# Kernel tuning notes

Hardware: AMD Instinct MI355X
Metric: run time of the kernel (lower is better)

## Reference

```python
import jax, jax.numpy as jnp
import numpy as np

B, S, D, HD, M, NH, DFF = 32, 512, 512, 512, 1000, 8, 2048
BETA = 0.5
DH = D // NH


def _make_seq(kt, km):
    # sorted event times, integer markers stored as floats (as in torch code);
    # last quarter of each sequence is padding with sentinel t = -1, marker = -1
    t = jnp.sort(jax.random.uniform(kt, (B, S)) * 100.0, axis=1)
    mk = jax.random.randint(km, (B, S), 0, M).astype(jnp.float32)
    valid = jnp.arange(S) < (3 * S // 4)
    t = jnp.where(valid, t, -1.0)
    mk = jnp.where(valid, mk, -1.0)
    return jnp.stack([t, mk], axis=-1)  # [B, S, 2]


def setup_inputs() -> dict:
    key = jax.random.key(0)
    ks = jax.random.split(key, 20)
    s = 0.02
    n = lambda k, shp: jax.random.normal(k, shp, dtype=jnp.float32) * s
    return {
        'x_H': _make_seq(ks[0], ks[1]),
        'x_F': _make_seq(ks[2], ks[3]),
        'W_m': n(ks[4], (D, M)),
        'W_t': n(ks[5], (D,)),
        'b_t': n(ks[6], (D,)),
        'Wq': n(ks[7], (D, D)),
        'Wk': n(ks[8], (D, D)),
        'Wv': n(ks[9], (D, D)),
        'Wo': n(ks[10], (D, D)),
        'W1': n(ks[11], (D, DFF)),
        'b1': jnp.zeros((DFF,), jnp.float32),
        'W2': n(ks[12], (DFF, D)),
        'b2': jnp.zeros((D,), jnp.float32),
        'Wp': n(ks[13], (D, HD)),
        'bp': jnp.zeros((HD,), jnp.float32),
        'W_out': n(ks[14], (2 * HD, M)),
        'b_out': jnp.zeros((M,), jnp.float32),
    }


def _embed(x, W_m, W_t, b_t):
    # out = beta * W_m[:, marker] + (1-beta) * (W_t * t + b_t); zeros when t < 0
    t = x[..., 0]                                         # [B, S]
    mk = jnp.clip(x[..., 1], 0, M - 1).astype(jnp.int32)  # [B, S]
    e = BETA * W_m.T[mk] + (1.0 - BETA) * (W_t * t[..., None] + b_t)
    return jnp.where((t >= 0)[..., None], e, 0.0), (t >= 0)


def _encoder(e, mask, Wq, Wk, Wv, Wo, W1, b1, W2, b2, Wp, bp):
    # masked multi-head self-attention encoder + masked mean pool -> [B, HD]
    q = (e @ Wq).reshape(B, S, NH, DH)
    k = (e @ Wk).reshape(B, S, NH, DH)
    v = (e @ Wv).reshape(B, S, NH, DH)
    scores = jnp.einsum('bqhd,bkhd->bhqk', q, k) / (DH ** 0.5)
    scores = jnp.where(mask[:, None, None, :], scores, -1e9)
    a = jax.nn.softmax(scores, axis=-1)
    o = jnp.einsum('bhqk,bkhd->bqhd', a, v).reshape(B, S, D) @ Wo
    h = e + o
    h = h + jax.nn.relu(h @ W1 + b1) @ W2 + b2
    mf = mask.astype(e.dtype)[..., None]
    pooled = (h * mf).sum(axis=1) / jnp.maximum(mf.sum(axis=1), 1.0)
    return pooled @ Wp + bp


def reference(x_H, x_F, W_m, W_t, b_t, Wq, Wk, Wv, Wo, W1, b1, W2, b2, Wp, bp, W_out, b_out):
    eH, mH = _embed(x_H, W_m, W_t, b_t)
    eF, mF = _embed(x_F, W_m, W_t, b_t)
    hH = _encoder(eH, mH, Wq, Wk, Wv, Wo, W1, b1, W2, b2, Wp, bp)
    hF = _encoder(eF, mF, Wq, Wk, Wv, Wo, W1, b1, W2, b2, Wp, bp)
    lam = jax.nn.softmax(jnp.concatenate([hH, hF], axis=1) @ W_out + b_out, axis=1)
    mu = jnp.argmax(lam, axis=1)
    return lam, mu
```

## Files before the change

kernel.cpp:

```cpp
#include <hip/hip_runtime.h>
#include <math.h>

#define BATCH 32
#define BB    64
#define SEQ  512
#define DIM  512
#define MM   1000
#define NHEAD 8
#define DHEAD 64
#define DFFN 2048
#define BROWS (BB * SEQ)

typedef __attribute__((ext_vector_type(8))) short short8;
typedef __attribute__((ext_vector_type(4))) float f32x4;

__device__ __forceinline__ ushort f2bf(float x) {
    unsigned u = __builtin_bit_cast(unsigned, x);
    unsigned r = (u + 0x7FFFu + ((u >> 16) & 1u)) >> 16;
    return (ushort)r;
}
__device__ __forceinline__ float bf2f(ushort h) {
    unsigned u = ((unsigned)h) << 16;
    return __builtin_bit_cast(float, u);
}

#define GL2LDS(g, s) __builtin_amdgcn_global_load_lds( \
    (const __attribute__((address_space(1))) unsigned int*)(g), \
    (__attribute__((address_space(3))) unsigned int*)(s), 16, 0, 0)

constexpr size_t OFF_WMT  = 0;
constexpr size_t OFF_MASK = 524288;
constexpr size_t OFF_POOL = 557056;
constexpr size_t OFF_HENC = 589824;
constexpr size_t OFF_LOG  = 622592;
constexpr size_t OFF_WQTH = 655360;
constexpr size_t OFF_W1TH = 1179648;
constexpr size_t OFF_W2TH = 1703936;
constexpr size_t OFF_EHI  = 2228224;
constexpr size_t OFF_ELO  = 10616832;
constexpr size_t OFF_QB   = 19005440;
constexpr size_t OFF_KB   = 27394048;
constexpr size_t OFF_VB   = 35782656;

__global__ __launch_bounds__(256)
void transpose_wm(const float* __restrict__ Wm, float* __restrict__ WmT)
{
    __shared__ float tile[32][33];
    int tx = threadIdx.x & 31;
    int ty = threadIdx.x >> 5;
    int mx = blockIdx.x * 32;
    int dy = blockIdx.y * 32;
    for (int i = ty; i < 32; i += 8) {
        int d = dy + i, m = mx + tx;
        tile[i][tx] = (m < MM) ? Wm[(size_t)d * MM + m] : 0.f;
    }
    __syncthreads();
    for (int i = ty; i < 32; i += 8) {
        int m = mx + i, d = dy + tx;
        if (m < MM) WmT[(size_t)m * DIM + d] = tile[tx][i];
    }
}

__global__ __launch_bounds__(256)
void split_wT4(const float* __restrict__ Wq, const float* __restrict__ Wk,
               const float* __restrict__ Wv, const float* __restrict__ Wo,
               ushort* __restrict__ Th)
{
    __shared__ float tile[32][33];
    int tx = threadIdx.x & 31;
    int ty = threadIdx.x >> 5;
    int n0 = blockIdx.x * 32;
    int k0 = blockIdx.y * 32;
    const float* W = (n0 < 512) ? Wq : (n0 < 1024) ? Wk
                   : (n0 < 1536) ? Wv : Wo;
    int nc = n0 & 511;
    for (int i = ty; i < 32; i += 8)
        tile[i][tx] = W[(size_t)(k0 + i) * 512 + nc + tx];
    __syncthreads();
    for (int i = ty; i < 32; i += 8)
        Th[(size_t)(n0 + i) * 512 + k0 + tx] = f2bf(tile[tx][i]);
}

__global__ __launch_bounds__(256)
void split_wT(const float* __restrict__ W, ushort* __restrict__ Th, int K, int N)
{
    __shared__ float tile[32][33];
    int tx = threadIdx.x & 31;
    int ty = threadIdx.x >> 5;
    int n0 = blockIdx.x * 32;
    int k0 = blockIdx.y * 32;
    for (int i = ty; i < 32; i += 8)
        tile[i][tx] = W[(size_t)(k0 + i) * N + n0 + tx];
    __syncthreads();
    for (int i = ty; i < 32; i += 8)
        Th[(size_t)(n0 + i) * K + k0 + tx] = f2bf(tile[tx][i]);
}

__global__ __launch_bounds__(256)
void embed_kernel(const float* __restrict__ xH, const float* __restrict__ xF,
                  const float* __restrict__ WmT, const float* __restrict__ Wt,
                  const float* __restrict__ bt,
                  ushort* __restrict__ ehi, ushort* __restrict__ elo,
                  float* __restrict__ maskA)
{
    int sub  = threadIdx.x >> 6;
    int lane = threadIdx.x & 63;
    int bs   = blockIdx.x * 4 + sub;
    const float* xp = (bs < BATCH * SEQ) ? (xH + (size_t)bs * 2)
                                         : (xF + (size_t)(bs - BATCH * SEQ) * 2);
    float t   = xp[0];
    float mkf = xp[1];
    int   mk  = (int)fminf(fmaxf(mkf, 0.f), (float)(MM - 1));
    bool  valid = (t >= 0.f);
    if (lane == 0) maskA[bs] = valid ? 1.f : 0.f;
    const float* wrow = WmT + (size_t)mk * DIM + lane * 8;
    float4 w0 = *reinterpret_cast<const float4*>(wrow);
    float4 w1 = *reinterpret_cast<const float4*>(wrow + 4);
    float4 t0 = *reinterpret_cast<const float4*>(Wt + lane * 8);
    float4 t1 = *reinterpret_cast<const float4*>(Wt + lane * 8 + 4);
    float4 b0 = *reinterpret_cast<const float4*>(bt + lane * 8);
    float4 b1 = *reinterpret_cast<const float4*>(bt + lane * 8 + 4);
    float v[8];
    v[0] = w0.x * 0.5f + 0.5f * (t0.x * t + b0.x);
    v[1] = w0.y * 0.5f + 0.5f * (t0.y * t + b0.y);
    v[2] = w0.z * 0.5f + 0.5f * (t0.z * t + b0.z);
    v[3] = w0.w * 0.5f + 0.5f * (t0.w * t + b0.w);
    v[4] = w1.x * 0.5f + 0.5f * (t1.x * t + b1.x);
    v[5] = w1.y * 0.5f + 0.5f * (t1.y * t + b1.y);
    v[6] = w1.z * 0.5f + 0.5f * (t1.z * t + b1.z);
    v[7] = w1.w * 0.5f + 0.5f * (t1.w * t + b1.w);
    union { uint4 u; ushort s[8]; } ph, pl;
    #pragma unroll
    for (int j = 0; j < 8; ++j) {
        float vv = valid ? v[j] : 0.f;
        ushort h = f2bf(vv);
        ph.s[j] = h;
        pl.s[j] = f2bf(vv - bf2f(h));
    }
    size_t base = (size_t)bs * DIM + lane * 8;
    *reinterpret_cast<uint4*>(ehi + base) = ph.u;
    *reinterpret_cast<uint4*>(elo + base) = pl.u;
}

template<int SEGS, bool BIAS, bool RELU, bool RES, bool PAIR, bool TOUT, bool TRIPLE>
__global__ __launch_bounds__(256)
void gemm_bf16(const ushort* __restrict__ A0, const ushort* __restrict__ A1,
               const ushort* __restrict__ B0, const ushort* __restrict__ B1,
               const float* __restrict__ bias,
               const ushort* __restrict__ Rh, const ushort* __restrict__ Rl,
               ushort* __restrict__ Oh, ushort* __restrict__ Ol,
               ushort* __restrict__ Ot,
               int Md, int Nd, int Kd, int lda, int ldb,
               const float* __restrict__ mrow)
{
    __shared__ __align__(16) ushort As[2][128 * 64];
    __shared__ __align__(16) ushort Bs[2][128 * 64];
    const int tid = threadIdx.x;
    const int w = tid >> 6, l = tid & 63;
    const int wr = w >> 1, wc = w & 1;
    const int l15 = l & 15, lg = l >> 4;
    const int id  = blockIdx.x + gridDim.x * blockIdx.y;
    const int nwg = gridDim.x * gridDim.y;
    const int qc  = nwg >> 3;
    const int lin = (id & 7) * qc + (id >> 3);
    const int row0 = (lin / gridDim.x) * 128;
    const int col0 = (lin % gridDim.x) * 128;
    const int lrow   = l >> 3;
    const int gchunk = (l & 7) ^ lrow;

    if (mrow) {
        float mv = (tid < 128) ? mrow[row0 + tid] : 0.f;
        if (!__syncthreads_or(mv != 0.f)) return;
    }

    f32x4 acc[4][4];
    #pragma unroll
    for (int m = 0; m < 4; m++)
        #pragma unroll
        for (int n = 0; n < 4; n++)
            acc[m][n] = (f32x4){0.f, 0.f, 0.f, 0.f};

    const int NT = SEGS * (Kd >> 6);
    int sseg = 0, skt = 0;

    auto stage = [&](int bi) {
        const ushort* Ap = (sseg == 1) ? A1 : A0;
        const ushort* Bp = (sseg == 2) ? B1 : B0;
        ushort* Asb = &As[bi][0];
        ushort* Bsb = &Bs[bi][0];
        #pragma unroll
        for (int r = 0; r < 4; ++r) {
            int rowb = w * 32 + r * 8;
            int row  = rowb + lrow;
            GL2LDS(Ap + (size_t)(row0 + row) * lda + skt + gchunk * 8,
                   Asb + rowb * 64);
            GL2LDS(Bp + (size_t)(col0 + row) * ldb + skt + gchunk * 8,
                   Bsb + rowb * 64);
        }
        skt += 64;
        if (skt == Kd) { skt = 0; ++sseg; }
    };

    stage(0);
    __syncthreads();

    for (int t = 0; t < NT; ++t) {
        const int cur = t & 1;
        if (t + 1 < NT) stage(cur ^ 1);
        const char* AsB = (const char*)&As[cur][0];
        const char* BsB = (const char*)&Bs[cur][0];
        #pragma unroll
        for (int ks = 0; ks < 2; ++ks) {
            const int g = ks * 4 + lg;
            short8 af[4], bfr[4];
            #pragma unroll
            for (int m = 0; m < 4; ++m) {
                int row = wr * 64 + m * 16 + l15;
                af[m] = *reinterpret_cast<const short8*>(
                    AsB + row * 128 + ((g ^ (row & 7)) << 4));
            }
            #pragma unroll
            for (int n = 0; n < 4; ++n) {
                int row = wc * 64 + n * 16 + l15;
                bfr[n] = *reinterpret_cast<const short8*>(
                    BsB + row * 128 + ((g ^ (row & 7)) << 4));
            }
            #pragma unroll
            for (int m = 0; m < 4; ++m)
                #pragma unroll
                for (int n = 0; n < 4; ++n)
                    acc[m][n] = __builtin_amdgcn_mfma_f32_16x16x32_bf16(
                        af[m], bfr[n], acc[m][n], 0, 0, 0);
        }
        __syncthreads();
    }

    #pragma unroll
    for (int m = 0; m < 4; ++m) {
        #pragma unroll
        for (int n = 0; n < 4; ++n) {
            int col = col0 + wc * 64 + n * 16 + l15;
            if (TRIPLE) {
                if (col0 < 512) {
                    #pragma unroll
                    for (int j = 0; j < 4; ++j) {
                        int row = row0 + wr * 64 + m * 16 + lg * 4 + j;
                        Oh[(size_t)row * 512 + col] = f2bf(acc[m][n][j]);
                    }
                } else if (col0 < 1024) {
                    #pragma unroll
                    for (int j = 0; j < 4; ++j) {
                        int row = row0 + wr * 64 + m * 16 + lg * 4 + j;
                        Ol[(size_t)row * 512 + (col - 512)] = f2bf(acc[m][n][j]);
                    }
                } else {
                    union { uint2 u; ushort s4[4]; } pk;
                    #pragma unroll
                    for (int j = 0; j < 4; ++j) pk.s4[j] = f2bf(acc[m][n][j]);
                    int brow = row0 + wr * 64 + m * 16 + lg * 4;
                    size_t idx = ((size_t)(brow >> 9) << 18)
                               + (size_t)(col - 1024) * SEQ + (brow & 511);
                    *reinterpret_cast<uint2*>(Ot + idx) = pk.u;
                }
            } else if (TOUT) {
                union { uint2 u; ushort s4[4]; } pk;
                #pragma unroll
                for (int j = 0; j < 4; ++j) pk.s4[j] = f2bf(acc[m][n][j]);
                int brow = row0 + wr * 64 + m * 16 + lg * 4;
                size_t idx = ((size_t)(brow >> 9) << 18) + (size_t)col * SEQ + (brow & 511);
                *reinterpret_cast<uint2*>(Oh + idx) = pk.u;
            } else {
                float bia = 0.f;
                if (BIAS) bia = bias[col];
                #pragma unroll
                for (int j = 0; j < 4; ++j) {
                    int row = row0 + wr * 64 + m * 16 + lg * 4 + j;
                    size_t idx = (size_t)row * Nd + col;
                    float v = acc[m][n][j] + bia;
                    if (RES)  v += bf2f(Rh[idx]) + bf2f(Rl[idx]);
                    if (RELU) v = fmaxf(v, 0.f);
                    ushort hv = f2bf(v);
                    Oh[idx] = hv;
                    if (PAIR) Ol[idx] = f2bf(v - bf2f(hv));
                }
            }
        }
    }
}

__global__ __launch_bounds__(512)
void attn_mfma(ushort* __restrict__ QO, const ushort* __restrict__ K,
               const ushort* __restrict__ Vt, const float* __restrict__ maskA)
{
    __shared__ __align__(16) ushort Ks[128 * 64];
    __shared__ __align__(16) ushort Vs[2][64 * 64];
    __shared__ __align__(16) ushort Pl[8][16 * 64];
    __shared__ float ms[128];
    const int h   = blockIdx.x;
    const int b   = blockIdx.y;
    const int qt  = blockIdx.z;
    const int tid = threadIdx.x;
    const int w = tid >> 6, l = tid & 63;
    const int l15 = l & 15, lg = l >> 4, l7 = l & 7;
    const int lrow   = l >> 3;
    const int gchunk = (l & 7) ^ lrow;
    const int qbase = qt * 128;

    {
        float qm = (tid < 128) ? maskA[b * SEQ + qbase + tid] : 0.f;
        if (!__syncthreads_or(qm != 0.f)) return;
    }

    ushort* Qs = &Pl[0][0];
    #pragma unroll
    for (int rr = 0; rr < 2; ++rr) {
        int rowb = rr * 64 + w * 8;
        int q = rowb + lrow;
        GL2LDS(QO + ((size_t)(b * SEQ + qbase + q)) * DIM + h * DHEAD + gchunk * 8,
               &Qs[rowb * 64]);
    }
    __syncthreads();

    short8 af[2];
    #pragma unroll
    for (int s = 0; s < 2; ++s) {
        int q = w * 16 + l15;
        int c = (s * 4 + lg) ^ l7;
        af[s] = *reinterpret_cast<const short8*>(&Qs[q * 64 + c * 8]);
    }

    f32x4 oacc[4];
    #pragma unroll
    for (int t = 0; t < 4; ++t) oacc[t] = (f32x4){0.f, 0.f, 0.f, 0.f};
    float lrun[4];
    #pragma unroll
    for (int j = 0; j < 4; ++j) lrun[j] = 0.f;

    ushort* pw = &Pl[w][0];

    for (int kv0 = 0; kv0 < SEQ; kv0 += 128) {
        float mv = (tid < 128) ? maskA[b * SEQ + kv0 + tid] : 0.f;
        int have = __syncthreads_or(mv != 0.f);
        if (tid < 128) ms[tid] = mv;
        if (!have) continue;

        #pragma unroll
        for (int rr = 0; rr < 2; ++rr) {
            int rowb = rr * 64 + w * 8;
            GL2LDS(K + ((size_t)(b * SEQ + kv0 + rowb + lrow)) * DIM
                     + h * DHEAD + gchunk * 8,
                   &Ks[rowb * 64]);
        }
        #pragma unroll
        for (int hf = 0; hf < 2; ++hf) {
            int rowb = w * 8;
            int row = rowb + lrow;
            GL2LDS(Vt + ((size_t)b << 18) + (size_t)(h * DHEAD + row) * SEQ
                      + kv0 + hf * 64 + gchunk * 8,
                   &Vs[hf][rowb * 64]);
        }
        __syncthreads();

        f32x4 sacc[8];
        #pragma unroll
        for (int t = 0; t < 8; ++t) sacc[t] = (f32x4){0.f, 0.f, 0.f, 0.f};
        #pragma unroll
        for (int s = 0; s < 2; ++s) {
            int c = (s * 4 + lg) ^ l7;
            #pragma unroll
            for (int t = 0; t < 8; ++t) {
                int kv = t * 16 + l15;
                short8 bf = *reinterpret_cast<const short8*>(&Ks[kv * 64 + c * 8]);
                sacc[t] = __builtin_amdgcn_mfma_f32_16x16x32_bf16(af[s], bf, sacc[t], 0, 0, 0);
            }
        }

        float mk[8];
        #pragma unroll
        for (int t = 0; t < 8; ++t) mk[t] = ms[t * 16 + l15];
        #pragma unroll
        for (int t = 0; t < 8; ++t)
            #pragma unroll
            for (int j = 0; j < 4; ++j)
                sacc[t][j] = mk[t] * __expf(sacc[t][j] * 0.125f);
        #pragma unroll
        for (int j = 0; j < 4; ++j) {
            float ps = (((sacc[0][j] + sacc[1][j]) + (sacc[2][j] + sacc[3][j]))
                      + ((sacc[4][j] + sacc[5][j]) + (sacc[6][j] + sacc[7][j])));
            ps += __shfl_xor(ps, 1);
            ps += __shfl_xor(ps, 2);
            ps += __shfl_xor(ps, 4);
            ps += __shfl_xor(ps, 8);
            lrun[j] += ps;
        }

        #pragma unroll
        for (int hf = 0; hf < 2; ++hf) {
            #pragma unroll
            for (int tt = 0; tt < 4; ++tt) {
                #pragma unroll
                for (int j = 0; j < 4; ++j) {
                    int qrow = lg * 4 + j;
                    int kvh = tt * 16 + l15;
                    int phys = qrow * 64 + (kvh & 7) + ((((kvh >> 3) ^ (qrow & 7))) << 3);
                    pw[phys] = f2bf(sacc[hf * 4 + tt][j]);
                }
            }
            #pragma unroll
            for (int s = 0; s < 2; ++s) {
                int c = (s * 4 + lg) ^ l7;
                short8 pa = *reinterpret_cast<const short8*>(&pw[l15 * 64 + c * 8]);
                #pragma unroll
                for (int t = 0; t < 4; ++t) {
                    int dh = t * 16 + l15;
                    short8 vb = *reinterpret_cast<const short8*>(&Vs[hf][dh * 64 + c * 8]);
                    oacc[t] = __builtin_amdgcn_mfma_f32_16x16x32_bf16(pa, vb, oacc[t], 0, 0, 0);
                }
            }
        }
    }

    float inv[4];
    #pragma unroll
    for (int j = 0; j < 4; ++j) inv[j] = 1.0f / lrun[j];
    #pragma unroll
    for (int t = 0; t < 4; ++t) {
        #pragma unroll
        for (int j = 0; j < 4; ++j) {
            size_t g = ((size_t)(b * SEQ + qbase + w * 16 + lg * 4 + j)) * DIM
                     + h * DHEAD + t * 16 + l15;
            QO[g] = f2bf(oacc[t][j] * inv[j]);
        }
    }
}

__global__ __launch_bounds__(512)
void pool_kernel(const ushort* __restrict__ hh, const ushort* __restrict__ hl,
                 const float* __restrict__ maskA, float* __restrict__ pooled)
{
    int b  = blockIdx.x;
    int dq = blockIdx.y;
    int dl = threadIdx.x & 31;
    int sg = threadIdx.x >> 5;
    int d  = dq * 64 + dl * 2;
    float a0 = 0.f, a1 = 0.f, cnt = 0.f;
    for (int s = sg; s < SEQ; s += 16) {
        float mv = maskA[b * SEQ + s];
        if (mv == 0.f) continue;
        size_t idx = ((size_t)(b * SEQ + s)) * DIM + d;
        unsigned vh = *reinterpret_cast<const unsigned*>(&hh[idx]);
        unsigned vl = *reinterpret_cast<const unsigned*>(&hl[idx]);
        a0 += bf2f((ushort)(vh & 0xffff)) + bf2f((ushort)(vl & 0xffff));
        a1 += bf2f((ushort)(vh >> 16))    + bf2f((ushort)(vl >> 16));
        cnt += 1.f;
    }
    __shared__ float r0[16][32];
    __shared__ float r1[16][32];
    __shared__ float rc[16];
    r0[sg][dl] = a0;
    r1[sg][dl] = a1;
    if (dl == 0) rc[sg] = cnt;
    __syncthreads();
    if (sg == 0) {
        float t0 = 0.f, t1 = 0.f, c = 0.f;
        #pragma unroll
        for (int g = 0; g < 16; ++g) { t0 += r0[g][dl]; t1 += r1[g][dl]; c += rc[g]; }
        float invc = 1.0f / fmaxf(c, 1.f);
        pooled[b * DIM + d]     = t0 * invc;
        pooled[b * DIM + d + 1] = t1 * invc;
    }
}

__global__ __launch_bounds__(512)
void proj_kernel(const float* __restrict__ pooled, const float* __restrict__ Wp,
                 const float* __restrict__ bp, float* __restrict__ henc)
{
    int b = blockIdx.x;
    int j = threadIdx.x;
    __shared__ float p[DIM];
    p[j] = pooled[b * DIM + j];
    __syncthreads();
    float a0 = 0.f, a1 = 0.f, a2 = 0.f, a3 = 0.f;
    for (int d = 0; d < DIM; d += 4) {
        a0 += p[d]     * Wp[(size_t)d       * DIM + j];
        a1 += p[d + 1] * Wp[(size_t)(d + 1) * DIM + j];
        a2 += p[d + 2] * Wp[(size_t)(d + 2) * DIM + j];
        a3 += p[d + 3] * Wp[(size_t)(d + 3) * DIM + j];
    }
    henc[(size_t)b * DIM + j] = ((a0 + a1) + (a2 + a3)) + bp[j];
}

__global__ __launch_bounds__(256)
void logits_kernel(const float* __restrict__ henc, const float* __restrict__ Wout,
                   const float* __restrict__ bout, float* __restrict__ logits)
{
    int b = blockIdx.y;
    int m = blockIdx.x * 256 + threadIdx.x;
    __shared__ float hh[2 * DIM];
    for (int j = threadIdx.x; j < DIM; j += 256) {
        hh[j]       = henc[(size_t)b * DIM + j];
        hh[DIM + j] = henc[(size_t)(BATCH + b) * DIM + j];
    }
    __syncthreads();
    if (m < MM) {
        float a0 = 0.f, a1 = 0.f, a2 = 0.f, a3 = 0.f;
        for (int j = 0; j < 2 * DIM; j += 4) {
            a0 += hh[j]     * Wout[(size_t)j       * MM + m];
            a1 += hh[j + 1] * Wout[(size_t)(j + 1) * MM + m];
            a2 += hh[j + 2] * Wout[(size_t)(j + 2) * MM + m];
            a3 += hh[j + 3] * Wout[(size_t)(j + 3) * MM + m];
        }
        logits[b * MM + m] = ((a0 + a1) + (a2 + a3)) + bout[m];
    }
}

__global__ __launch_bounds__(256)
void smax_kernel(const float* __restrict__ logits, float* __restrict__ out)
{
    int b   = blockIdx.x;
    int tid = threadIdx.x;
    __shared__ float red[256];
    __shared__ int   redi[256];

    float v[4];
    float mx = -INFINITY;
    #pragma unroll
    for (int i = 0; i < 4; i++) {
        int m = tid + i * 256;
        if (m < MM) { v[i] = logits[b * MM + m]; mx = fmaxf(mx, v[i]); }
        else v[i] = -INFINITY;
    }
    red[tid] = mx; __syncthreads();
    for (int st = 128; st > 0; st >>= 1) {
        if (tid < st) red[tid] = fmaxf(red[tid], red[tid + st]);
        __syncthreads();
    }
    mx = red[0]; __syncthreads();

    float sum = 0.f;
    #pragma unroll
    for (int i = 0; i < 4; i++) {
        int m = tid + i * 256;
        if (m < MM) { v[i] = expf(v[i] - mx); sum += v[i]; }
    }
    red[tid] = sum; __syncthreads();
    for (int st = 128; st > 0; st >>= 1) {
        if (tid < st) red[tid] += red[tid + st];
        __syncthreads();
    }
    float inv = 1.0f / red[0]; __syncthreads();

    float bestv = -INFINITY; int besti = 0x7fffffff;
    #pragma unroll
    for (int i = 0; i < 4; i++) {
        int m = tid + i * 256;
        if (m < MM) {
            float lam = v[i] * inv;
            out[b * MM + m] = lam;
            if (lam > bestv) { bestv = lam; besti = m; }
        }
    }
    red[tid] = bestv; redi[tid] = besti; __syncthreads();
    for (int st = 128; st > 0; st >>= 1) {
        if (tid < st) {
            float ov = red[tid + st]; int oi = redi[tid + st];
            if (ov > red[tid] || (ov == red[tid] && oi < redi[tid])) {
                red[tid] = ov; redi[tid] = oi;
            }
        }
        __syncthreads();
    }
    if (tid == 0) out[BATCH * MM + b] = (float)redi[0];
}

extern "C" void kernel_launch(void* const* d_in, const int* in_sizes, int n_in,
                              void* d_out, int out_size, void* d_ws, size_t ws_size,
                              hipStream_t stream)
{
    const float* xH   = (const float*)d_in[0];
    const float* xF   = (const float*)d_in[1];
    const float* Wm   = (const float*)d_in[2];
    const float* Wt   = (const float*)d_in[3];
    const float* bt   = (const float*)d_in[4];
    const float* Wq   = (const float*)d_in[5];
    const float* Wk   = (const float*)d_in[6];
    const float* Wv   = (const float*)d_in[7];
    const float* Wo   = (const float*)d_in[8];
    const float* W1   = (const float*)d_in[9];
    const float* b1   = (const float*)d_in[10];
    const float* W2   = (const float*)d_in[11];
    const float* b2   = (const float*)d_in[12];
    const float* Wp   = (const float*)d_in[13];
    const float* bp   = (const float*)d_in[14];
    const float* Wout = (const float*)d_in[15];
    const float* bout = (const float*)d_in[16];
    float* out = (float*)d_out;

    float* ws     = (float*)d_ws;
    float*  WmT    = ws + OFF_WMT;
    float*  maskA  = ws + OFF_MASK;
    float*  pooled = ws + OFF_POOL;
    float*  henc   = ws + OFF_HENC;
    float*  logits = ws + OFF_LOG;
    ushort* WqkvTh = (ushort*)(ws + OFF_WQTH);
    ushort* WoTh   = WqkvTh + (size_t)1536 * 512;
    ushort* W1Th   = (ushort*)(ws + OFF_W1TH);
    ushort* W2Th   = (ushort*)(ws + OFF_W2TH);
    ushort* ehi    = (ushort*)(ws + OFF_EHI);
    ushort* elo    = (ushort*)(ws + OFF_ELO);
    ushort* Qb     = (ushort*)(ws + OFF_QB);
    ushort* Kb     = (ushort*)(ws + OFF_KB);
    ushort* Vtb    = (ushort*)(ws + OFF_VB);
    ushort* rbuf   = (ushort*)(ws + OFF_VB);

    transpose_wm<<<dim3(32, 16), 256, 0, stream>>>(Wm, WmT);
    split_wT4<<<dim3(64, 16), 256, 0, stream>>>(Wq, Wk, Wv, Wo, WqkvTh);
    split_wT<<<dim3(64, 16), 256, 0, stream>>>(W1, W1Th, DIM, DFFN);
    split_wT<<<dim3(16, 64), 256, 0, stream>>>(W2, W2Th, DFFN, DIM);

    embed_kernel<<<dim3(BROWS / 4), 256, 0, stream>>>(
        xH, xF, WmT, Wt, bt, ehi, elo, maskA);
    gemm_bf16<1,false,false,false,false,false,true><<<dim3(12, 256), 256, 0, stream>>>(
        ehi, nullptr, WqkvTh, nullptr, nullptr, nullptr, nullptr,
        Qb, Kb, Vtb, BROWS, 512, DIM, DIM, DIM, maskA);
    attn_mfma<<<dim3(NHEAD, BB, 4), 512, 0, stream>>>(Qb, Kb, Vtb, maskA);
    gemm_bf16<1,false,false,true,true,false,false><<<dim3(4, 256), 256, 0, stream>>>(
        Qb, nullptr, WoTh, nullptr, nullptr, ehi, elo,
        ehi, elo, nullptr, BROWS, DIM, DIM, DIM, DIM, maskA);
    for (int nc = 0; nc < 2; nc++) {
        gemm_bf16<1,true,true,false,false,false,false><<<dim3(8, 256), 256, 0, stream>>>(
            ehi, nullptr, W1Th + (size_t)nc * 1024 * DIM, nullptr,
            b1 + nc * 1024, nullptr, nullptr,
            rbuf, nullptr, nullptr, BROWS, 1024, DIM, DIM, DIM, maskA);
        if (nc == 0)
            gemm_bf16<1,true,false,true,true,false,false><<<dim3(4, 256), 256, 0, stream>>>(
                rbuf, nullptr, W2Th, nullptr, b2, ehi, elo,
                Qb, Kb, nullptr, BROWS, DIM, 1024, 1024, DFFN, maskA);
        else
            gemm_bf16<1,false,false,true,true,false,false><<<dim3(4, 256), 256, 0, stream>>>(
                rbuf, nullptr, W2Th + 1024, nullptr, nullptr, Qb, Kb,
                Qb, Kb, nullptr, BROWS, DIM, 1024, 1024, DFFN, maskA);
    }
    pool_kernel<<<dim3(BB, 8), 512, 0, stream>>>(Qb, Kb, maskA, pooled);
    proj_kernel<<<dim3(BB), 512, 0, stream>>>(pooled, Wp, bp, henc);

    logits_kernel<<<dim3(4, BATCH), 256, 0, stream>>>(henc, Wout, bout, logits);
    smax_kernel<<<dim3(BATCH), 256, 0, stream>>>(logits, out);
}
```

Measured before the change: 425.4 us.

## Double-buffer attention KV tiles, merge weight-prep kernels, fuse logits with softmax

Three unrelated changes. The attention kernel now streams K/V in 64-row tiles through two LDS buffers, prefetching the next non-empty tile while computing the current one, and precomputes a bitmask of fully masked tiles so they are skipped. Four weight transpose/convert kernels become one launch split by block index, and the logits GEMV is fused into the softmax/argmax kernel. The merges cut launch count, but the fused head runs only 32 blocks, which may serialize the Wout GEMV.

Result: slower. 492.1 us (+15.7%).

```diff
diff --git a/kernel.cpp b/kernel.cpp
--- a/kernel.cpp
+++ b/kernel.cpp
@@ -32,7 +32,6 @@
 constexpr size_t OFF_MASK = 524288;
 constexpr size_t OFF_POOL = 557056;
 constexpr size_t OFF_HENC = 589824;
-constexpr size_t OFF_LOG  = 622592;
 constexpr size_t OFF_WQTH = 655360;
 constexpr size_t OFF_W1TH = 1179648;
 constexpr size_t OFF_W2TH = 1703936;
@@ -43,57 +42,56 @@
 constexpr size_t OFF_VB   = 35782656;
 
 __global__ __launch_bounds__(256)
-void transpose_wm(const float* __restrict__ Wm, float* __restrict__ WmT)
+void setup_all(const float* __restrict__ Wm,
+               const float* __restrict__ Wq, const float* __restrict__ Wk,
+               const float* __restrict__ Wv, const float* __restrict__ Wo,
+               const float* __restrict__ W1, const float* __restrict__ W2,
+               float* __restrict__ WmT, ushort* __restrict__ WqkvTh,
+               ushort* __restrict__ W1Th, ushort* __restrict__ W2Th)
 {
     __shared__ float tile[32][33];
-    int tx = threadIdx.x & 31;
-    int ty = threadIdx.x >> 5;
-    int mx = blockIdx.x * 32;
-    int dy = blockIdx.y * 32;
-    for (int i = ty; i < 32; i += 8) {
-        int d = dy + i, m = mx + tx;
-        tile[i][tx] = (m < MM) ? Wm[(size_t)d * MM + m] : 0.f;
-    }
-    __syncthreads();
-    for (int i = ty; i < 32; i += 8) {
-        int m = mx + i, d = dy + tx;
-        if (m < MM) WmT[(size_t)m * DIM + d] = tile[tx][i];
-    }
-}
-
-__global__ __launch_bounds__(256)
-void split_wT4(const float* __restrict__ Wq, const float* __restrict__ Wk,
-               const float* __restrict__ Wv, const float* __restrict__ Wo,
-               ushort* __restrict__ Th)
-{
-    __shared__ float tile[32][33];
-    int tx = threadIdx.x & 31;
-    int ty = threadIdx.x >> 5;
-    int n0 = blockIdx.x * 32;
-    int k0 = blockIdx.y * 32;
-    const float* W = (n0 < 512) ? Wq : (n0 < 1024) ? Wk
-                   : (n0 < 1536) ? Wv : Wo;
-    int nc = n0 & 511;
-    for (int i = ty; i < 32; i += 8)
-        tile[i][tx] = W[(size_t)(k0 + i) * 512 + nc + tx];
-    __syncthreads();
-    for (int i = ty; i < 32; i += 8)
-        Th[(size_t)(n0 + i) * 512 + k0 + tx] = f2bf(tile[tx][i]);
-}
-
-__global__ __launch_bounds__(256)
-void split_wT(const float* __restrict__ W, ushort* __restrict__ Th, int K, int N)
-{
-    __shared__ float tile[32][33];
-    int tx = threadIdx.x & 31;
-    int ty = threadIdx.x >> 5;
-    int n0 = blockIdx.x * 32;
-    int k0 = blockIdx.y * 32;
-    for (int i = ty; i < 32; i += 8)
-        tile[i][tx] = W[(size_t)(k0 + i) * N + n0 + tx];
-    __syncthreads();
-    for (int i = ty; i < 32; i += 8)
-        Th[(size_t)(n0 + i) * K + k0 + tx] = f2bf(tile[tx][i]);
+    const int bid = blockIdx.x;
+    const int tx = threadIdx.x & 31;
+    const int ty = threadIdx.x >> 5;
+    if (bid < 512) {
+        int mx = (bid & 31) * 32, dy = (bid >> 5) * 32;
+        for (int i = ty; i < 32; i += 8) {
+            int d = dy + i, m = mx + tx;
+            tile[i][tx] = (m < MM) ? Wm[(size_t)d * MM + m] : 0.f;
+        }
+        __syncthreads();
+        for (int i = ty; i < 32; i += 8) {
+            int m = mx + i, d = dy + tx;
+            if (m < MM) WmT[(size_t)m * DIM + d] = tile[tx][i];
+        }
+    } else if (bid < 1536) {
+        int id = bid - 512;
+        int n0 = (id & 63) * 32, k0 = (id >> 6) * 32;
+        const float* W = (n0 < 512) ? Wq : (n0 < 1024) ? Wk
+                       : (n0 < 1536) ? Wv : Wo;
+        int nc = n0 & 511;
+        for (int i = ty; i < 32; i += 8)
+            tile[i][tx] = W[(size_t)(k0 + i) * 512 + nc + tx];
+        __syncthreads();
+        for (int i = ty; i < 32; i += 8)
+            WqkvTh[(size_t)(n0 + i) * 512 + k0 + tx] = f2bf(tile[tx][i]);
+    } else if (bid < 2560) {
+        int id = bid - 1536;
+        int n0 = (id & 63) * 32, k0 = (id >> 6) * 32;
+        for (int i = ty; i < 32; i += 8)
+            tile[i][tx] = W1[(size_t)(k0 + i) * DFFN + n0 + tx];
+        __syncthreads();
+        for (int i = ty; i < 32; i += 8)
+            W1Th[(size_t)(n0 + i) * DIM + k0 + tx] = f2bf(tile[tx][i]);
+    } else {
+        int id = bid - 2560;
+        int n0 = (id & 15) * 32, k0 = (id >> 4) * 32;
+        for (int i = ty; i < 32; i += 8)
+            tile[i][tx] = W2[(size_t)(k0 + i) * DIM + n0 + tx];
+        __syncthreads();
+        for (int i = ty; i < 32; i += 8)
+            W2Th[(size_t)(n0 + i) * DFFN + k0 + tx] = f2bf(tile[tx][i]);
+    }
 }
 
 __global__ __launch_bounds__(256)
@@ -292,10 +290,10 @@
 void attn_mfma(ushort* __restrict__ QO, const ushort* __restrict__ K,
                const ushort* __restrict__ Vt, const float* __restrict__ maskA)
 {
-    __shared__ __align__(16) ushort Ks[128 * 64];
+    __shared__ __align__(16) ushort Ks[2][64 * 64];
     __shared__ __align__(16) ushort Vs[2][64 * 64];
     __shared__ __align__(16) ushort Pl[8][16 * 64];
-    __shared__ float ms[128];
+    __shared__ float ms[512];
     const int h   = blockIdx.x;
     const int b   = blockIdx.y;
     const int qt  = blockIdx.z;
@@ -306,27 +304,30 @@
     const int gchunk = (l & 7) ^ lrow;
     const int qbase = qt * 128;
 
-    {
-        float qm = (tid < 128) ? maskA[b * SEQ + qbase + tid] : 0.f;
-        if (!__syncthreads_or(qm != 0.f)) return;
-    }
-
-    ushort* Qs = &Pl[0][0];
     #pragma unroll
     for (int rr = 0; rr < 2; ++rr) {
         int rowb = rr * 64 + w * 8;
-        int q = rowb + lrow;
-        GL2LDS(QO + ((size_t)(b * SEQ + qbase + q)) * DIM + h * DHEAD + gchunk * 8,
-               &Qs[rowb * 64]);
-    }
-    __syncthreads();
+        GL2LDS(QO + ((size_t)(b * SEQ + qbase + rowb + lrow)) * DIM
+                  + h * DHEAD + gchunk * 8,
+               &Pl[0][0] + rowb * 64);
+    }
+    ms[tid] = maskA[b * SEQ + tid];
+    float qm = (tid < 128) ? maskA[b * SEQ + qbase + tid] : 0.f;
+    if (!__syncthreads_or(qm != 0.f)) return;
+
+    unsigned hbits = 0;
+    #pragma unroll
+    for (int t = 0; t < 8; ++t) {
+        int mine = (tid < 64) ? (ms[t * 64 + tid] != 0.f) : 0;
+        if (__syncthreads_or(mine)) hbits |= (1u << t);
+    }
 
     short8 af[2];
     #pragma unroll
     for (int s = 0; s < 2; ++s) {
         int q = w * 16 + l15;
         int c = (s * 4 + lg) ^ l7;
-        af[s] = *reinterpret_cast<const short8*>(&Qs[q * 64 + c * 8]);
+        af[s] = *reinterpret_cast<const short8*>(&Pl[0][0] + q * 64 + c * 8);
     }
 
     f32x4 oacc[4];
@@ -338,55 +339,52 @@
 
     ushort* pw = &Pl[w][0];
 
-    for (int kv0 = 0; kv0 < SEQ; kv0 += 128) {
-        float mv = (tid < 128) ? maskA[b * SEQ + kv0 + tid] : 0.f;
-        int have = __syncthreads_or(mv != 0.f);
-        if (tid < 128) ms[tid] = mv;
-        if (!have) continue;
-
-        #pragma unroll
-        for (int rr = 0; rr < 2; ++rr) {
-            int rowb = rr * 64 + w * 8;
-            GL2LDS(K + ((size_t)(b * SEQ + kv0 + rowb + lrow)) * DIM
-                     + h * DHEAD + gchunk * 8,
-                   &Ks[rowb * 64]);
-        }
-        #pragma unroll
-        for (int hf = 0; hf < 2; ++hf) {
-            int rowb = w * 8;
-            int row = rowb + lrow;
-            GL2LDS(Vt + ((size_t)b << 18) + (size_t)(h * DHEAD + row) * SEQ
-                      + kv0 + hf * 64 + gchunk * 8,
-                   &Vs[hf][rowb * 64]);
-        }
-        __syncthreads();
-
-        f32x4 sacc[8];
-        #pragma unroll
-        for (int t = 0; t < 8; ++t) sacc[t] = (f32x4){0.f, 0.f, 0.f, 0.f};
+    auto stagekv = [&](int t, int bi) {
+        int kv0 = t * 64;
+        GL2LDS(K + ((size_t)(b * SEQ + kv0 + w * 8 + lrow)) * DIM
+                 + h * DHEAD + gchunk * 8,
+               &Ks[bi][0] + w * 8 * 64);
+        GL2LDS(Vt + ((size_t)b << 18) + (size_t)(h * DHEAD + w * 8 + lrow) * SEQ
+                  + kv0 + gchunk * 8,
+               &Vs[bi][0] + w * 8 * 64);
+    };
+
+    int t0 = 0;
+    while (t0 < 8 && !(hbits & (1u << t0))) ++t0;
+    stagekv(t0, 0);
+    __syncthreads();
+    int cur = 0;
+    for (int t = t0; t < 8; ) {
+        int tn = t + 1;
+        while (tn < 8 && !(hbits & (1u << tn))) ++tn;
+        if (tn < 8) stagekv(tn, cur ^ 1);
+
+        f32x4 sacc[4];
+        #pragma unroll
+        for (int t4 = 0; t4 < 4; ++t4) sacc[t4] = (f32x4){0.f, 0.f, 0.f, 0.f};
         #pragma unroll
         for (int s = 0; s < 2; ++s) {
             int c = (s * 4 + lg) ^ l7;
             #pragma unroll
-            for (int t = 0; t < 8; ++t) {
-                int kv = t * 16 + l15;
-                short8 bf = *reinterpret_cast<const short8*>(&Ks[kv * 64 + c * 8]);
-                sacc[t] = __builtin_amdgcn_mfma_f32_16x16x32_bf16(af[s], bf, sacc[t], 0, 0, 0);
-            }
-        }
-
-        float mk[8];
-        #pragma unroll
-        for (int t = 0; t < 8; ++t) mk[t] = ms[t * 16 + l15];
-        #pragma unroll
-        for (int t = 0; t < 8; ++t)
+            for (int t4 = 0; t4 < 4; ++t4) {
+                int kv = t4 * 16 + l15;
+                short8 bf = *reinterpret_cast<const short8*>(
+                    &Ks[cur][0] + kv * 64 + c * 8);
+                sacc[t4] = __builtin_amdgcn_mfma_f32_16x16x32_bf16(af[s], bf, sacc[t4], 0, 0, 0);
+            }
+        }
+
+        float mk[4];
+        #pragma unroll
+        for (int t4 = 0; t4 < 4; ++t4) mk[t4] = ms[t * 64 + t4 * 16 + l15];
+        #pragma unroll
+        for (int t4 = 0; t4 < 4; ++t4)
             #pragma unroll
             for (int j = 0; j < 4; ++j)
-                sacc[t][j] = mk[t] * __expf(sacc[t][j] * 0.125f);
+                sacc[t4][j] = mk[t4] * __expf(sacc[t4][j] * 0.125f);
         #pragma unroll
         for (int j = 0; j < 4; ++j) {
-            float ps = (((sacc[0][j] + sacc[1][j]) + (sacc[2][j] + sacc[3][j]))
-                      + ((sacc[4][j] + sacc[5][j]) + (sacc[6][j] + sacc[7][j])));
+            float ps = (sacc[0][j] + sacc[1][j]) + (sacc[2][j] + sacc[3][j]);
             ps += __shfl_xor(ps, 1);
             ps += __shfl_xor(ps, 2);
             ps += __shfl_xor(ps, 4);
@@ -395,29 +393,32 @@
         }
 
         #pragma unroll
-        for (int hf = 0; hf < 2; ++hf) {
+        for (int t4 = 0; t4 < 4; ++t4) {
             #pragma unroll
-            for (int tt = 0; tt < 4; ++tt) {
-                #pragma unroll
-                for (int j = 0; j < 4; ++j) {
-                    int qrow = lg * 4 + j;
-                    int kvh = tt * 16 + l15;
-                    int phys = qrow * 64 + (kvh & 7) + ((((kvh >> 3) ^ (qrow & 7))) << 3);
-                    pw[phys] = f2bf(sacc[hf * 4 + tt][j]);
-                }
-            }
+            for (int j = 0; j < 4; ++j) {
+                int qrow = lg * 4 + j;
+                int kvh = t4 * 16 + l15;
+                int phys = qrow * 64 + (kvh & 7) + ((((kvh >> 3) ^ (qrow & 7))) << 3);
+                pw[phys] = f2bf(sacc[t4][j]);
+            }
+        }
+
+        #pragma unroll
+        for (int s = 0; s < 2; ++s) {
+            int c = (s * 4 + lg) ^ l7;
+            short8 pa = *reinterpret_cast<const short8*>(&pw[l15 * 64 + c * 8]);
             #pragma unroll
-            for (int s = 0; s < 2; ++s) {
-                int c = (s * 4 + lg) ^ l7;
-                short8 pa = *reinterpret_cast<const short8*>(&pw[l15 * 64 + c * 8]);
-                #pragma unroll
-                for (int t = 0; t < 4; ++t) {
-                    int dh = t * 16 + l15;
-                    short8 vb = *reinterpret_cast<const short8*>(&Vs[hf][dh * 64 + c * 8]);
-                    oacc[t] = __builtin_amdgcn_mfma_f32_16x16x32_bf16(pa, vb, oacc[t], 0, 0, 0);
-                }
-            }
-        }
+            for (int dt = 0; dt < 4; ++dt) {
+                int dh = dt * 16 + l15;
+                short8 vb = *reinterpret_cast<const short8*>(
+                    &Vs[cur][0] + dh * 64 + c * 8);
+                oacc[dt] = __builtin_amdgcn_mfma_f32_16x16x32_bf16(pa, vb, oacc[dt], 0, 0, 0);
+            }
+        }
+
+        __syncthreads();
+        cur ^= 1;
+        t = tn;
     }
 
     float inv[4];
@@ -491,44 +492,36 @@
 }
 
 __global__ __launch_bounds__(256)
-void logits_kernel(const float* __restrict__ henc, const float* __restrict__ Wout,
-                   const float* __restrict__ bout, float* __restrict__ logits)
-{
-    int b = blockIdx.y;
-    int m = blockIdx.x * 256 + threadIdx.x;
+void head_kernel(const float* __restrict__ henc, const float* __restrict__ Wout,
+                 const float* __restrict__ bout, float* __restrict__ out)
+{
+    int b   = blockIdx.x;
+    int tid = threadIdx.x;
     __shared__ float hh[2 * DIM];
-    for (int j = threadIdx.x; j < DIM; j += 256) {
+    __shared__ float red[256];
+    __shared__ int   redi[256];
+    for (int j = tid; j < DIM; j += 256) {
         hh[j]       = henc[(size_t)b * DIM + j];
         hh[DIM + j] = henc[(size_t)(BATCH + b) * DIM + j];
     }
     __syncthreads();
-    if (m < MM) {
-        float a0 = 0.f, a1 = 0.f, a2 = 0.f, a3 = 0.f;
-        for (int j = 0; j < 2 * DIM; j += 4) {
-            a0 += hh[j]     * Wout[(size_t)j       * MM + m];
-            a1 += hh[j + 1] * Wout[(size_t)(j + 1) * MM + m];
-            a2 += hh[j + 2] * Wout[(size_t)(j + 2) * MM + m];
-            a3 += hh[j + 3] * Wout[(size_t)(j + 3) * MM + m];
-        }
-        logits[b * MM + m] = ((a0 + a1) + (a2 + a3)) + bout[m];
-    }
-}
-
-__global__ __launch_bounds__(256)
-void smax_kernel(const float* __restrict__ logits, float* __restrict__ out)
-{
-    int b   = blockIdx.x;
-    int tid = threadIdx.x;
-    __shared__ float red[256];
-    __shared__ int   redi[256];
 
     float v[4];
     float mx = -INFINITY;
     #pragma unroll
-    for (int i = 0; i < 4; i++) {
+    for (int i = 0; i < 4; ++i) {
         int m = tid + i * 256;
-        if (m < MM) { v[i] = logits[b * MM + m]; mx = fmaxf(mx, v[i]); }
-        else v[i] = -INFINITY;
+        if (m < MM) {
+            float a0 = 0.f, a1 = 0.f, a2 = 0.f, a3 = 0.f;
+            for (int j = 0; j < 2 * DIM; j += 4) {
+                a0 += hh[j]     * Wout[(size_t)j       * MM + m];
+                a1 += hh[j + 1] * Wout[(size_t)(j + 1) * MM + m];
+                a2 += hh[j + 2] * Wout[(size_t)(j + 2) * MM + m];
+                a3 += hh[j + 3] * Wout[(size_t)(j + 3) * MM + m];
+            }
+            v[i] = ((a0 + a1) + (a2 + a3)) + bout[m];
+            mx = fmaxf(mx, v[i]);
+        } else v[i] = -INFINITY;
     }
     red[tid] = mx; __syncthreads();
     for (int st = 128; st > 0; st >>= 1) {
@@ -539,7 +532,7 @@
 
     float sum = 0.f;
     #pragma unroll
-    for (int i = 0; i < 4; i++) {
+    for (int i = 0; i < 4; ++i) {
         int m = tid + i * 256;
         if (m < MM) { v[i] = expf(v[i] - mx); sum += v[i]; }
     }
@@ -552,7 +545,7 @@
 
     float bestv = -INFINITY; int besti = 0x7fffffff;
     #pragma unroll
-    for (int i = 0; i < 4; i++) {
+    for (int i = 0; i < 4; ++i) {
         int m = tid + i * 256;
         if (m < MM) {
             float lam = v[i] * inv;
@@ -601,7 +594,6 @@
     float*  maskA  = ws + OFF_MASK;
     float*  pooled = ws + OFF_POOL;
     float*  henc   = ws + OFF_HENC;
-    float*  logits = ws + OFF_LOG;
     ushort* WqkvTh = (ushort*)(ws + OFF_WQTH);
     ushort* WoTh   = WqkvTh + (size_t)1536 * 512;
     ushort* W1Th   = (ushort*)(ws + OFF_W1TH);
@@ -613,10 +605,8 @@
     ushort* Vtb    = (ushort*)(ws + OFF_VB);
     ushort* rbuf   = (ushort*)(ws + OFF_VB);
 
-    transpose_wm<<<dim3(32, 16), 256, 0, stream>>>(Wm, WmT);
-    split_wT4<<<dim3(64, 16), 256, 0, stream>>>(Wq, Wk, Wv, Wo, WqkvTh);
-    split_wT<<<dim3(64, 16), 256, 0, stream>>>(W1, W1Th, DIM, DFFN);
-    split_wT<<<dim3(16, 64), 256, 0, stream>>>(W2, W2Th, DFFN, DIM);
+    setup_all<<<dim3(3584), 256, 0, stream>>>(
+        Wm, Wq, Wk, Wv, Wo, W1, W2, WmT, WqkvTh, W1Th, W2Th);
 
     embed_kernel<<<dim3(BROWS / 4), 256, 0, stream>>>(
         xH, xF, WmT, Wt, bt, ehi, elo, maskA);
@@ -643,7 +633,5 @@
     }
     pool_kernel<<<dim3(BB, 8), 512, 0, stream>>>(Qb, Kb, maskA, pooled);
     proj_kernel<<<dim3(BB), 512, 0, stream>>>(pooled, Wp, bp, henc);
-
-    logits_kernel<<<dim3(4, BATCH), 256, 0, stream>>>(henc, Wout, bout, logits);
-    smax_kernel<<<dim3(BATCH), 256, 0, stream>>>(logits, out);
-}
+    head_kernel<<<dim3(BATCH), 256, 0, stream>>>(henc, Wout, bout, out);
+}
```
